# Optimization experiments

Hardware: AMD Instinct MI355X
Metric: run time of the kernel (lower is better)

The kernel has to match this reference:

```python
import jax, jax.numpy as jnp
import numpy as np

B, K, N, M = 4, 512, 4096, 4
CHI2_95 = 7.815   # chi-square df=3, q=0.95
JITTER = 1e-6
ALPHA = 1.5       # sigma_cover_alpha
SIG_FLOOR = 1e-3
SIG_CEIL = 100.0
BETA = 0.85       # beta_parent_sigma
SHRINK = 1.0      # parent_sigma_shrink
KNN = 8           # fps_knn


def _sym(A):
    return 0.5 * (A + jnp.swapaxes(A, -1, -2))


def _chol3(S, eps=1e-6):
    # manual 3x3 Cholesky (vectorized, never fails), mirrors _safe_cholesky_3x3_manual
    s00, s11, s22 = S[..., 0, 0], S[..., 1, 1], S[..., 2, 2]
    s01, s02, s12 = S[..., 0, 1], S[..., 0, 2], S[..., 1, 2]
    l00 = jnp.sqrt(jnp.clip(s00, eps))
    l10 = s01 / jnp.clip(l00, eps)
    l20 = s02 / jnp.clip(l00, eps)
    l11 = jnp.sqrt(jnp.clip(s11 - l10 ** 2, eps))
    l21 = (s12 - l20 * l10) / jnp.clip(l11, eps)
    l22 = jnp.sqrt(jnp.clip(s22 - l20 ** 2 - l21 ** 2, eps))
    zz = jnp.zeros_like(l00)
    return jnp.stack([jnp.stack([l00, zz, zz], -1),
                      jnp.stack([l10, l11, zz], -1),
                      jnp.stack([l20, l21, l22], -1)], -2)


def _allocate_quota(pi, n_total, mask):
    # vectorized version of _allocate_quota: floor + largest-remainder
    valid = mask > 0.5
    pi = jnp.where(valid, pi, 0.0)
    pi = pi / jnp.clip(jnp.sum(pi, -1, keepdims=True), 1e-9)
    raw = pi * float(n_total)
    base = jnp.floor(raw)
    rem = (float(n_total) - jnp.sum(base, -1)).astype(jnp.int32)          # [B]
    frac = jnp.where(valid, raw - base, -1e9)
    order = jnp.argsort(-frac, axis=-1)
    rank = jnp.argsort(order, axis=-1)
    n_k = base.astype(jnp.int32) + (rank < rem[:, None]).astype(jnp.int32)
    return jnp.where(valid, n_k, 0)


def setup_inputs() -> dict:
    key = jax.random.key(0)
    k1, k2, k3, k4 = jax.random.split(key, 4)
    mu_p = jax.random.normal(k1, (B, K, 3), jnp.float32) * 5.0
    A = jax.random.normal(k2, (B, K, 3, 3), jnp.float32)
    Sig_p = 0.1 * jnp.einsum('bkij,bklj->bkil', A, A) + 0.5 * jnp.eye(3, dtype=jnp.float32)
    occ = jax.random.uniform(k3, (B, K), jnp.float32) + 0.1
    mask_parent = jnp.ones((B, K), jnp.float32)
    node_mask = jnp.ones((B, N), jnp.float32)
    z = jax.random.normal(k4, (B, N, M, 3), jnp.float32)
    return {"mu_p": mu_p, "Sig_p": Sig_p, "occ": occ,
            "mask_parent": mask_parent, "node_mask": node_mask, "z": z}


def reference(mu_p, Sig_p, occ, mask_parent, node_mask, z):
    b, k, _ = mu_p.shape
    n = node_mask.shape[1]
    m = z.shape[2]
    I3 = jnp.eye(3, dtype=mu_p.dtype)

    # --- quota allocation ---
    pi = occ * (mask_parent > 0.5).astype(occ.dtype)
    n_k = _allocate_quota(pi, n, mask_parent)                              # [B,K]

    # --- child -> parent assignment (packed layout, replaces Python loops) ---
    csum = jnp.cumsum(n_k, -1)                                             # [B,K]
    ar = jnp.arange(n)
    parent_idx = jax.vmap(lambda c: jnp.searchsorted(c, ar, side='right'))(csum)
    parent_idx = jnp.clip(parent_idx, 0, k - 1)                            # [B,N]

    # --- sample inside parent ellipsoid (rejection-lite) ---
    Sig_s = _sym(Sig_p * SHRINK) + JITTER * I3
    mu_c = jax.vmap(lambda a, i: a[i])(mu_p, parent_idx)                   # [B,N,3]
    Sig_c = jax.vmap(lambda a, i: a[i])(Sig_s, parent_idx)                 # [B,N,3,3]
    L = _chol3(Sig_c)                                                      # [B,N,3,3]
    cand = mu_c[:, :, None, :] + jnp.einsum('bnij,bnmj->bnmi', L, z)       # [B,N,M,3]
    # delta = cand - mu = L z, so maha2 = z^T z exactly (as in the torch code)
    maha2 = jnp.sum(z * z, -1)                                             # [B,N,M]
    inside = maha2 <= CHI2_95
    # keep first inside candidate; else smallest maha2
    score = jnp.where(inside, jnp.arange(m, dtype=maha2.dtype), 1e6 + maha2)
    pick = jnp.argmin(score, axis=-1)                                      # [B,N]
    mu0 = jnp.take_along_axis(cand, pick[..., None, None], axis=2)[:, :, 0, :]
    mu0 = mu0 * node_mask[..., None]                                       # [B,N,3]

    # --- spacing-based Sigma (kNN mean distance, isotropic) ---
    sq = jnp.sum(mu0 * mu0, -1)
    d2 = sq[:, :, None] + sq[:, None, :] - 2.0 * jnp.einsum('bnd,bmd->bnm', mu0, mu0)
    pair_ok = (node_mask[:, :, None] > 0.5) & (node_mask[:, None, :] > 0.5)
    eye = jnp.eye(n, dtype=bool)
    d2 = jnp.where(pair_ok & ~eye, d2, 1e9)
    neg_top, _ = jax.lax.top_k(-d2, KNN)                                   # [B,N,KNN]
    d_mean = jnp.mean(jnp.sqrt(jnp.clip(-neg_top, 0.0)), -1)               # [B,N]
    sigma = jnp.clip(ALPHA * d_mean, SIG_FLOOR, SIG_CEIL)
    Sig_spacing = (sigma ** 2)[..., None, None] * I3 + JITTER * I3         # [B,N,3,3]

    # --- parent/spacing Sigma blend ---
    Sig_pc = jax.vmap(lambda a, i: a[i])(_sym(Sig_p), parent_idx)
    Sig_pc = _sym(Sig_pc) + JITTER * I3
    Sig0 = BETA * Sig_pc + (1.0 - BETA) * Sig_spacing
    Sig0 = _sym(Sig0) + JITTER * I3
    Sig0 = Sig0 * node_mask[:, :, None, None]
    return mu0, Sig0, parent_idx
```

## Files before the change

kernel.cpp:

```cpp
#include <hip/hip_runtime.h>
#include <math.h>

#define B_ 4
#define K_ 512
#define N_ 4096
#define M_ 4

#define KTHREADS 512
#define SLOTS 8
#define SEGS 64
#define ROWS 16
#define CHUNK 1024
#define NCHUNK (N_ / CHUNK)
#define BIGF 3.0e38f

#define CSW(x,y) { float _lo = fminf(x,y); y = fmaxf(x,y); x = _lo; }

#define SORT8S(s0,s1,s2,s3,s4,s5,s6,s7) \
    CSW(s0,s1) CSW(s2,s3) CSW(s4,s5) CSW(s6,s7) \
    CSW(s0,s2) CSW(s1,s3) CSW(s4,s6) CSW(s5,s7) \
    CSW(s1,s2) CSW(s5,s6) \
    CSW(s0,s4) CSW(s1,s5) CSW(s2,s6) CSW(s3,s7) \
    CSW(s2,s4) CSW(s3,s5) \
    CSW(s1,s2) CSW(s3,s4) CSW(s5,s6)

#define BMERGE8S(K0,K1,K2,K3,K4,K5,K6,K7, S0,S1,S2,S3,S4,S5,S6,S7) \
    K0 = fminf(K0,S7); K1 = fminf(K1,S6); K2 = fminf(K2,S5); K3 = fminf(K3,S4); \
    K4 = fminf(K4,S3); K5 = fminf(K5,S2); K6 = fminf(K6,S1); K7 = fminf(K7,S0); \
    CSW(K0,K4) CSW(K1,K5) CSW(K2,K6) CSW(K3,K7) \
    CSW(K0,K2) CSW(K1,K3) CSW(K4,K6) CSW(K5,K7) \
    CSW(K0,K1) CSW(K2,K3) CSW(K4,K5) CSW(K6,K7)

#define WMERGE(K0,K1,K2,K3,K4,K5,K6,K7, off) { \
    float _b0 = __shfl_xor(K0, off, 64); float _b1 = __shfl_xor(K1, off, 64); \
    float _b2 = __shfl_xor(K2, off, 64); float _b3 = __shfl_xor(K3, off, 64); \
    float _b4 = __shfl_xor(K4, off, 64); float _b5 = __shfl_xor(K5, off, 64); \
    float _b6 = __shfl_xor(K6, off, 64); float _b7 = __shfl_xor(K7, off, 64); \
    BMERGE8S(K0,K1,K2,K3,K4,K5,K6,K7, _b0,_b1,_b2,_b3,_b4,_b5,_b6,_b7) }

__global__ __launch_bounds__(512) void fused_kernel(const float* __restrict__ mu_p,
                                                    const float* __restrict__ Sig_p,
                                                    const float* __restrict__ occ,
                                                    const float* __restrict__ mask_parent,
                                                    const float* __restrict__ node_mask,
                                                    const float* __restrict__ z,
                                                    float* __restrict__ out,
                                                    float4* __restrict__ mu4,
                                                    int useF4)
{
    __shared__ double sh_a[K_];
    __shared__ double sh_part[32];
    __shared__ alignas(16) double sh_frac[K_];
    __shared__ alignas(16) float  sh_ffr[K_];
    __shared__ float  csf[K_];
    __shared__ double Lsh[K_][6];
    __shared__ int    sh_wsum[8];
    __shared__ double s_S;
    __shared__ int    s_rem;

    int b  = blockIdx.x >> 3;
    int rb = blockIdx.x & 7;
    int k  = threadIdx.x;

    float mk = mask_parent[b * K_ + k];
    bool valid = mk > 0.5f;
    double pi = valid ? (double)occ[b * K_ + k] : 0.0;
    sh_a[k] = pi;
    __syncthreads();

    if (k < 32) {
        const double* a = sh_a + (k >> 3) * 128;
        int j = k & 7;
        double r = a[j];
        for (int i = 8; i < 128; i += 8) r += a[j + i];
        sh_part[k] = r;
    }
    __syncthreads();
    if (k == 0) {
        double pw[4];
        #pragma unroll
        for (int blk = 0; blk < 4; ++blk) {
            const double* p = sh_part + blk * 8;
            pw[blk] = ((p[0]+p[1])+(p[2]+p[3]))+((p[4]+p[5])+(p[6]+p[7]));
        }
        s_S = fmax((pw[0]+pw[1])+(pw[2]+pw[3]), 1e-9);
    }
    __syncthreads();

    double raw  = (pi / s_S) * 4096.0;
    double base = floor(raw);
    double frac = valid ? (raw - base) : -1e9;
    sh_frac[k] = frac;
    sh_ffr[k]  = (float)frac;
    __syncthreads();
    sh_a[k] = base;
    __syncthreads();
    if (k < 32) {
        const double* a = sh_a + (k >> 3) * 128;
        int j = k & 7;
        double r = a[j];
        for (int i = 8; i < 128; i += 8) r += a[j + i];
        sh_part[k] = r;
    }
    __syncthreads();
    if (k == 0) {
        double pw[4];
        #pragma unroll
        for (int blk = 0; blk < 4; ++blk) {
            const double* p = sh_part + blk * 8;
            pw[blk] = ((p[0]+p[1])+(p[2]+p[3]))+((p[4]+p[5])+(p[6]+p[7]));
        }
        s_rem = (int)(4096.0 - ((pw[0]+pw[1])+(pw[2]+pw[3])));
    }
    __syncthreads();

    int nkv = 0;
    if (valid) {
        float fl = (float)frac;
        int rank = 0, eq = 0;
        const float4* f4 = reinterpret_cast<const float4*>(sh_ffr);
        #pragma unroll 4
        for (int j4 = 0; j4 < K_ / 4; ++j4) {
            float4 q = f4[j4];
            rank += (q.x > fl) ? 1 : 0;  eq += (q.x == fl) ? 1 : 0;
            rank += (q.y > fl) ? 1 : 0;  eq += (q.y == fl) ? 1 : 0;
            rank += (q.z > fl) ? 1 : 0;  eq += (q.z == fl) ? 1 : 0;
            rank += (q.w > fl) ? 1 : 0;  eq += (q.w == fl) ? 1 : 0;
        }
        if (__builtin_expect(eq != 1, 0)) {
            double f = frac;
            rank = 0;
            for (int j = 0; j < K_; ++j) {
                double fj = sh_frac[j];
                rank += ((fj > f) || (fj == f && j < k)) ? 1 : 0;
            }
        }
        nkv = (int)base + (rank < s_rem ? 1 : 0);
    }

    {
        int lane = k & 63;
        int w    = k >> 6;
        int v = nkv;
        #pragma unroll
        for (int off = 1; off < 64; off <<= 1) {
            int t = __shfl_up(v, off, 64);
            v += (lane >= off) ? t : 0;
        }
        if (lane == 63) sh_wsum[w] = v;
        __syncthreads();
        int woff = 0;
        #pragma unroll
        for (int i = 0; i < 7; ++i) woff += (i < w) ? sh_wsum[i] : 0;
        csf[k] = (float)(v + woff);
    }

    {
        const float* S = Sig_p + (size_t)(b * K_ + k) * 9;
        double s00 = (double)S[0] + 1e-6;
        double s01 = 0.5 * ((double)S[1] + (double)S[3]);
        double s02 = 0.5 * ((double)S[2] + (double)S[6]);
        double s11 = (double)S[4] + 1e-6;
        double s12 = 0.5 * ((double)S[5] + (double)S[7]);
        double s22 = (double)S[8] + 1e-6;

        const double eps = 1e-6;
        double l00 = sqrt(fmax(s00, eps));
        double l10 = s01 / fmax(l00, eps);
        double l20 = s02 / fmax(l00, eps);
        double l11 = sqrt(fmax(s11 - l10 * l10, eps));
        double l21 = (s12 - l20 * l10) / fmax(l11, eps);
        double l22 = sqrt(fmax(s22 - l20 * l20 - l21 * l21, eps));

        Lsh[k][0] = l00; Lsh[k][1] = l10; Lsh[k][2] = l20;
        Lsh[k][3] = l11; Lsh[k][4] = l21; Lsh[k][5] = l22;
    }
    __syncthreads();

    int n = rb * 512 + k;
    float nf = (float)n;
    int lo = 0, hi = K_;
    while (lo < hi) {
        int mid = (lo + hi) >> 1;
        if (csf[mid] <= nf) lo = mid + 1; else hi = mid;
    }
    int p = lo < (K_ - 1) ? lo : (K_ - 1);

    double l00 = Lsh[p][0], l10 = Lsh[p][1], l20 = Lsh[p][2];
    double l11 = Lsh[p][3], l21 = Lsh[p][4], l22 = Lsh[p][5];

    const float* zp = z + (size_t)(b * N_ + n) * (M_ * 3);
    double bestScore = 1e30;
    int pick = 0;
    #pragma unroll
    for (int m = 0; m < M_; ++m) {
        double z0 = (double)zp[m*3+0], z1 = (double)zp[m*3+1], z2 = (double)zp[m*3+2];
        double maha2 = (z0 * z0 + z1 * z1) + z2 * z2;
        double score = (maha2 <= 7.815) ? (double)m : (1e6 + maha2);
        if (score < bestScore) { bestScore = score; pick = m; }
    }

    double z0 = (double)zp[pick*3+0], z1 = (double)zp[pick*3+1], z2 = (double)zp[pick*3+2];
    const float* mu = mu_p + (size_t)(b * K_ + p) * 3;
    double nm = (double)node_mask[b * N_ + n];
    double c0 = ((double)mu[0] + ((l00 * z0)))                       * nm;
    double c1 = ((double)mu[1] + ((l10 * z0 + l11 * z1)))            * nm;
    double c2 = ((double)mu[2] + ((l20 * z0 + l21 * z1) + l22 * z2)) * nm;

    size_t o = (size_t)(b * N_ + n) * 3;
    float f0 = (float)c0, f1 = (float)c1, f2 = (float)c2;
    out[o + 0] = f0;
    out[o + 1] = f1;
    out[o + 2] = f2;
    if (useF4) {
        float sq = (f0 * f0 + f1 * f1) + f2 * f2;
        mu4[b * N_ + n] = make_float4(f0, f1, f2, sq);
    }
    out[(size_t)B_ * N_ * 12 + (size_t)(b * N_ + n)] = (float)p;
}

#define LD8_G(u) { \
    int col_ = colbase + u * SEGS + seg; \
    float4 q_ = cp[col_]; \
    f##u##x = q_.x; f##u##y = q_.y; f##u##z = q_.z; f##u##w = q_.w; }

#define LD8_S(u) { \
    int col_ = colbase + u * SEGS + seg; \
    size_t o_ = (size_t)(bN + col_) * 3; \
    f##u##x = mu0[o_]; f##u##y = mu0[o_+1]; f##u##z = mu0[o_+2]; \
    f##u##w = (f##u##x*f##u##x + f##u##y*f##u##y) + f##u##z*f##u##z; }

#define DIST2(u, SQ) \
    s##u = fmaf(a00, f##u##x, fmaf(a01, f##u##y, fmaf(a02, f##u##z, f##u##w))); \
    r##u = fmaf(a10, f##u##x, fmaf(a11, f##u##y, fmaf(a12, f##u##z, f##u##w))); \
    if (SQ) { int col_ = colbase + u * SEGS + seg; \
        s##u = (col_ == n0) ? BIGF : s##u; \
        r##u = (col_ == n1) ? BIGF : r##u; }

#define GROUP8V(LD, SQ) { \
    float f0x,f0y,f0z,f0w, f1x,f1y,f1z,f1w, f2x,f2y,f2z,f2w, f3x,f3y,f3z,f3w; \
    float f4x,f4y,f4z,f4w, f5x,f5y,f5z,f5w, f6x,f6y,f6z,f6w, f7x,f7y,f7z,f7w; \
    LD(0) LD(1) LD(2) LD(3) LD(4) LD(5) LD(6) LD(7) \
    float s0,s1,s2,s3,s4,s5,s6,s7, r0,r1,r2,r3,r4,r5,r6,r7; \
    DIST2(0,SQ) DIST2(1,SQ) DIST2(2,SQ) DIST2(3,SQ) \
    DIST2(4,SQ) DIST2(5,SQ) DIST2(6,SQ) DIST2(7,SQ) \
    SORT8S(s0,s1,s2,s3,s4,s5,s6,s7) \
    BMERGE8S(ka0,ka1,ka2,ka3,ka4,ka5,ka6,ka7, s0,s1,s2,s3,s4,s5,s6,s7) \
    SORT8S(r0,r1,r2,r3,r4,r5,r6,r7) \
    BMERGE8S(kb0,kb1,kb2,kb3,kb4,kb5,kb6,kb7, r0,r1,r2,r3,r4,r5,r6,r7) }

__global__ __launch_bounds__(KTHREADS, 4) void knn_kernel(const float* __restrict__ Sig_p,
                                                          const float* __restrict__ node_mask,
                                                          const float4* __restrict__ mu4,
                                                          int useF4,
                                                          float* __restrict__ out)
{
    __shared__ float  shk[ROWS][8 * 8 + 1];

    int b   = blockIdx.x / (N_ / ROWS);
    int rb  = blockIdx.x % (N_ / ROWS);
    int tid = threadIdx.x;
    int slot = tid & (SLOTS - 1);
    int seg  = tid >> 3;

    const float* mu0 = out;
    const float4* cp = mu4 + (size_t)b * N_;
    int bN = b * N_;
    int n0 = rb * ROWS + slot;
    int n1 = n0 + SLOTS;

    float x0, y0, z0v, x1, y1, z1v;
    if (useF4) {
        float4 p0 = cp[n0]; x0 = p0.x; y0 = p0.y; z0v = p0.z;
        float4 p1 = cp[n1]; x1 = p1.x; y1 = p1.y; z1v = p1.z;
    } else {
        size_t so0 = (size_t)(bN + n0) * 3;
        size_t so1 = (size_t)(bN + n1) * 3;
        x0 = mu0[so0]; y0 = mu0[so0+1]; z0v = mu0[so0+2];
        x1 = mu0[so1]; y1 = mu0[so1+1]; z1v = mu0[so1+2];
    }
    float a00 = -2.0f*x0, a01 = -2.0f*y0, a02 = -2.0f*z0v;
    float a10 = -2.0f*x1, a11 = -2.0f*y1, a12 = -2.0f*z1v;

    float ka0=BIGF,ka1=BIGF,ka2=BIGF,ka3=BIGF,ka4=BIGF,ka5=BIGF,ka6=BIGF,ka7=BIGF;
    float kb0=BIGF,kb1=BIGF,kb2=BIGF,kb3=BIGF,kb4=BIGF,kb5=BIGF,kb6=BIGF,kb7=BIGF;

    int selfc = (rb * ROWS) >> 10;

    if (useF4) {
        #pragma unroll
        for (int c = 0; c < NCHUNK; ++c) {
            if (c == selfc) {
                { int colbase = c * CHUNK;       GROUP8V(LD8_G, 1) }
                { int colbase = c * CHUNK + 512; GROUP8V(LD8_G, 1) }
            } else {
                { int colbase = c * CHUNK;       GROUP8V(LD8_G, 0) }
                { int colbase = c * CHUNK + 512; GROUP8V(LD8_G, 0) }
            }
        }
    } else {
        #pragma unroll
        for (int c = 0; c < NCHUNK; ++c) {
            if (c == selfc) {
                { int colbase = c * CHUNK;       GROUP8V(LD8_S, 1) }
                { int colbase = c * CHUNK + 512; GROUP8V(LD8_S, 1) }
            } else {
                { int colbase = c * CHUNK;       GROUP8V(LD8_S, 0) }
                { int colbase = c * CHUNK + 512; GROUP8V(LD8_S, 0) }
            }
        }
    }

    WMERGE(ka0,ka1,ka2,ka3,ka4,ka5,ka6,ka7, 8)
    WMERGE(ka0,ka1,ka2,ka3,ka4,ka5,ka6,ka7, 16)
    WMERGE(ka0,ka1,ka2,ka3,ka4,ka5,ka6,ka7, 32)
    WMERGE(kb0,kb1,kb2,kb3,kb4,kb5,kb6,kb7, 8)
    WMERGE(kb0,kb1,kb2,kb3,kb4,kb5,kb6,kb7, 16)
    WMERGE(kb0,kb1,kb2,kb3,kb4,kb5,kb6,kb7, 32)

    int lane = tid & 63;
    int w    = tid >> 6;
    if (lane < SLOTS) {
        shk[lane][w*8+0] = ka0; shk[lane][w*8+1] = ka1;
        shk[lane][w*8+2] = ka2; shk[lane][w*8+3] = ka3;
        shk[lane][w*8+4] = ka4; shk[lane][w*8+5] = ka5;
        shk[lane][w*8+6] = ka6; shk[lane][w*8+7] = ka7;
        shk[lane+SLOTS][w*8+0] = kb0; shk[lane+SLOTS][w*8+1] = kb1;
        shk[lane+SLOTS][w*8+2] = kb2; shk[lane+SLOTS][w*8+3] = kb3;
        shk[lane+SLOTS][w*8+4] = kb4; shk[lane+SLOTS][w*8+5] = kb5;
        shk[lane+SLOTS][w*8+6] = kb6; shk[lane+SLOTS][w*8+7] = kb7;
    }
    __syncthreads();

    if (tid < ROWS) {
        int r = tid;
        int nn = rb * ROWS + r;
        float e0=BIGF,e1=BIGF,e2=BIGF,e3=BIGF,e4=BIGF,e5=BIGF,e6=BIGF,e7=BIGF;
        #pragma unroll
        for (int w2 = 0; w2 < 8; ++w2) {
            float b0 = shk[r][w2*8+0], b1 = shk[r][w2*8+1];
            float b2 = shk[r][w2*8+2], b3 = shk[r][w2*8+3];
            float b4 = shk[r][w2*8+4], b5 = shk[r][w2*8+5];
            float b6 = shk[r][w2*8+6], b7 = shk[r][w2*8+7];
            BMERGE8S(e0,e1,e2,e3,e4,e5,e6,e7, b0,b1,b2,b3,b4,b5,b6,b7)
        }

        float cn;
        if (useF4) {
            cn = cp[nn].w;
        } else {
            size_t so = (size_t)(bN + nn) * 3;
            float xx = mu0[so], yy = mu0[so+1], zz = mu0[so+2];
            cn = (xx*xx + yy*yy) + zz*zz;
        }

        double s0 = sqrt(fmax((double)(cn + e0), 0.0)), s1 = sqrt(fmax((double)(cn + e1), 0.0));
        double s2 = sqrt(fmax((double)(cn + e2), 0.0)), s3 = sqrt(fmax((double)(cn + e3), 0.0));
        double s4 = sqrt(fmax((double)(cn + e4), 0.0)), s5 = sqrt(fmax((double)(cn + e5), 0.0));
        double s6 = sqrt(fmax((double)(cn + e6), 0.0)), s7 = sqrt(fmax((double)(cn + e7), 0.0));
        double d_mean = (((s0 + s1) + (s2 + s3)) + ((s4 + s5) + (s6 + s7))) / 8.0;

        double sigma = fmin(fmax(1.5 * d_mean, 1e-3), 100.0);
        double spacing = sigma * sigma + 1e-6;

        int p = (int)out[(size_t)B_ * N_ * 12 + (size_t)(bN + nn)];
        const float* S = Sig_p + (size_t)(b * K_ + p) * 9;
        double s00 = (double)S[0];
        double s01 = 0.5 * ((double)S[1] + (double)S[3]);
        double s02 = 0.5 * ((double)S[2] + (double)S[6]);
        double s11 = (double)S[4];
        double s12 = 0.5 * ((double)S[5] + (double)S[7]);
        double s22 = (double)S[8];

        const double BETA = 0.85;
        const double OMB  = 1.0 - 0.85;
        double nm = (double)node_mask[bN + nn];

        double d00 = (BETA * (s00 + 1e-6) + OMB * spacing) + 1e-6;
        double d11 = (BETA * (s11 + 1e-6) + OMB * spacing) + 1e-6;
        double d22 = (BETA * (s22 + 1e-6) + OMB * spacing) + 1e-6;
        double o01 = BETA * s01;
        double o02 = BETA * s02;
        double o12 = BETA * s12;

        float* Sg = out + (size_t)B_ * N_ * 3 + (size_t)(bN + nn) * 9;
        Sg[0] = (float)(d00 * nm); Sg[1] = (float)(o01 * nm); Sg[2] = (float)(o02 * nm);
        Sg[3] = (float)(o01 * nm); Sg[4] = (float)(d11 * nm); Sg[5] = (float)(o12 * nm);
        Sg[6] = (float)(o02 * nm); Sg[7] = (float)(o12 * nm); Sg[8] = (float)(d22 * nm);
    }
}

extern "C" void kernel_launch(void* const* d_in, const int* in_sizes, int n_in,
                              void* d_out, int out_size, void* d_ws, size_t ws_size,
                              hipStream_t stream)
{
    const float* mu_p        = (const float*)d_in[0];
    const float* Sig_p       = (const float*)d_in[1];
    const float* occ         = (const float*)d_in[2];
    const float* mask_parent = (const float*)d_in[3];
    const float* node_mask   = (const float*)d_in[4];
    const float* z           = (const float*)d_in[5];
    float* out = (float*)d_out;

    int useF4 = (ws_size >= (size_t)B_ * N_ * sizeof(float4)) ? 1 : 0;
    float4* mu4 = (float4*)d_ws;

    fused_kernel<<<B_ * 8, 512, 0, stream>>>(mu_p, Sig_p, occ, mask_parent,
                                             node_mask, z, out, mu4, useF4);
    knn_kernel<<<B_ * (N_ / ROWS), KTHREADS, 0, stream>>>(Sig_p, node_mask,
                                                          mu4, useF4, out);
}
```

Measured before the change: 47.70 us.

## Stage candidate points through double-buffered LDS chunks with register prefetch

The kNN kernel now copies each 1024-point chunk of packed candidate points into a double-buffered shared-memory array. While the current chunk is processed, the next chunk is prefetched into registers and then written to the other buffer, followed by a barrier. Previously each thread read candidates straight from global memory (mostly L2/L1 hits, since every thread in the block reads the same data). The change trades global/L1 traffic for LDS reads, but adds 32KB of LDS per block and a barrier per chunk, which may reduce occupancy.

```diff
diff --git a/kernel.cpp b/kernel.cpp
--- a/kernel.cpp
+++ b/kernel.cpp
@@ -219,9 +219,8 @@
     out[(size_t)B_ * N_ * 12 + (size_t)(b * N_ + n)] = (float)p;
 }
 
-#define LD8_G(u) { \
-    int col_ = colbase + u * SEGS + seg; \
-    float4 q_ = cp[col_]; \
+#define LD8_L(u) { \
+    float4 q_ = lbuf[u * SEGS + seg]; \
     f##u##x = q_.x; f##u##y = q_.y; f##u##z = q_.z; f##u##w = q_.w; }
 
 #define LD8_S(u) { \
@@ -249,12 +248,29 @@
     SORT8S(r0,r1,r2,r3,r4,r5,r6,r7) \
     BMERGE8S(kb0,kb1,kb2,kb3,kb4,kb5,kb6,kb7, r0,r1,r2,r3,r4,r5,r6,r7) }
 
+#define CHUNK_STEP(c, cur, nxt, LAST) { \
+    float4 st0, st1; \
+    if (!(LAST)) { st0 = cp[(c+1)*CHUNK + tid]; st1 = cp[(c+1)*CHUNK + 512 + tid]; } \
+    if ((c) == selfc) { \
+        { int colbase = (c)*CHUNK;       const float4* lbuf = chk[cur];       GROUP8V(LD8_L, 1) } \
+        { int colbase = (c)*CHUNK + 512; const float4* lbuf = chk[cur] + 512; GROUP8V(LD8_L, 1) } \
+    } else { \
+        { int colbase = (c)*CHUNK;       const float4* lbuf = chk[cur];       GROUP8V(LD8_L, 0) } \
+        { int colbase = (c)*CHUNK + 512; const float4* lbuf = chk[cur] + 512; GROUP8V(LD8_L, 0) } \
+    } \
+    if (!(LAST)) { \
+        chk[nxt][tid]       = st0; \
+        chk[nxt][tid + 512] = st1; \
+        __syncthreads(); \
+    } }
+
 __global__ __launch_bounds__(KTHREADS, 4) void knn_kernel(const float* __restrict__ Sig_p,
                                                           const float* __restrict__ node_mask,
                                                           const float4* __restrict__ mu4,
                                                           int useF4,
                                                           float* __restrict__ out)
 {
+    __shared__ float4 chk[2][CHUNK];
     __shared__ float  shk[ROWS][8 * 8 + 1];
 
     int b   = blockIdx.x / (N_ / ROWS);
@@ -288,16 +304,14 @@
     int selfc = (rb * ROWS) >> 10;
 
     if (useF4) {
-        #pragma unroll
-        for (int c = 0; c < NCHUNK; ++c) {
-            if (c == selfc) {
-                { int colbase = c * CHUNK;       GROUP8V(LD8_G, 1) }
-                { int colbase = c * CHUNK + 512; GROUP8V(LD8_G, 1) }
-            } else {
-                { int colbase = c * CHUNK;       GROUP8V(LD8_G, 0) }
-                { int colbase = c * CHUNK + 512; GROUP8V(LD8_G, 0) }
-            }
-        }
+        chk[0][tid]       = cp[tid];
+        chk[0][tid + 512] = cp[tid + 512];
+        __syncthreads();
+
+        CHUNK_STEP(0, 0, 1, 0)
+        CHUNK_STEP(1, 1, 0, 0)
+        CHUNK_STEP(2, 0, 1, 0)
+        CHUNK_STEP(3, 1, 0, 1)
     } else {
         #pragma unroll
         for (int c = 0; c < NCHUNK; ++c) {
```

Measured after the change: 48.88 us. +2.5%, slower.
